# Kernel optimization log

Hardware: AMD Instinct MI355X
Metric: run time of the kernel (lower is better)

The kernel has to match this reference:

```python
import jax, jax.numpy as jnp
import numpy as np

B, T, D, HD, HN, O = 32, 512, 512, 64, 16, 512
EPS = 1e-5


def setup_inputs() -> dict:
    key = jax.random.key(0)
    ks = jax.random.split(key, 12)
    s = lambda fan_in: 1.0 / np.sqrt(fan_in)
    inp = {
        "inputs": jax.random.normal(ks[0], (B, T, D), dtype=jnp.float32),
        "Wq": jax.random.uniform(ks[1], (HN, D, HD), jnp.float32, -s(D), s(D)),
        "bq": jnp.zeros((HN, HD), jnp.float32),
        "Wk": jax.random.uniform(ks[2], (HN, D, HD), jnp.float32, -s(D), s(D)),
        "bk": jnp.zeros((HN, HD), jnp.float32),
        "Wv": jax.random.uniform(ks[3], (HN, D, HD), jnp.float32, -s(D), s(D)),
        "bv": jnp.zeros((HN, HD), jnp.float32),
        "Wr": jax.random.uniform(ks[4], (D, O), jnp.float32, -s(D), s(D)),
        "br": jnp.zeros((O,), jnp.float32),
        "Wo": jax.random.uniform(ks[5], (HN * HD, O), jnp.float32, -s(HN * HD), s(HN * HD)),
        "bo": jnp.zeros((O,), jnp.float32),
        "ln1_w": jnp.ones((O,), jnp.float32),
        "ln1_b": jnp.zeros((O,), jnp.float32),
        "Wfc": jax.random.uniform(ks[6], (O, O), jnp.float32, -s(O), s(O)),
        "bfc": jnp.zeros((O,), jnp.float32),
        "ln2_w": jnp.ones((O,), jnp.float32),
        "ln2_b": jnp.zeros((O,), jnp.float32),
    }
    return inp


def _layernorm(x, w, b):
    mu = jnp.mean(x, axis=-1, keepdims=True)
    var = jnp.mean(jnp.square(x - mu), axis=-1, keepdims=True)
    return (x - mu) * jax.lax.rsqrt(var + EPS) * w + b


def reference(inputs, Wq, bq, Wk, bk, Wv, bv, Wr, br, Wo, bo,
              ln1_w, ln1_b, Wfc, bfc, ln2_w, ln2_b):
    # causal mask: multiply-then-subtract as in the original
    score_mask = jnp.tril(jnp.ones((T, T), jnp.float32))        # [T,T]
    padding_mask = (score_mask == 0).astype(jnp.float32) * 1e9  # [T,T]

    residual = inputs @ Wr + br                                  # [B,T,O]

    # batched per-head projections with nonstandard activations
    q = jax.nn.relu(jnp.einsum('btd,hdf->bhtf', inputs, Wq) + bq[None, :, None, :])
    k = jax.nn.relu(jnp.einsum('btd,hdf->bhtf', inputs, Wk) + bk[None, :, None, :])
    v = jnp.tanh(jnp.einsum('btd,hdf->bhtf', inputs, Wv) + bv[None, :, None, :])

    scores = jnp.einsum('bhtf,bhsf->bhts', q, k) / jnp.sqrt(jnp.float32(HD))
    scores = scores * score_mask - padding_mask                  # [B,H,T,T]
    weights = jax.nn.softmax(scores, axis=-1)
    heads = jnp.einsum('bhts,bhsf->bhtf', weights, v)            # [B,H,T,HD]

    # concat heads (head order preserved) + tanh output projection
    concat = heads.transpose(0, 2, 1, 3).reshape(B, T, HN * HD)
    out = jnp.tanh(concat @ Wo + bo)                             # [B,T,O]

    out = _layernorm(out + residual, ln1_w, ln1_b)
    fc = jax.nn.relu(out @ Wfc + bfc)
    out = _layernorm(fc + out, ln2_w, ln2_b)
    return out
```

## Files before the change

### kernel.cpp

```cpp
#include <hip/hip_runtime.h>
#include <hip/hip_bf16.h>

#define B_  32
#define T_  512
#define D_  512
#define HD_ 64
#define HN_ 16
#define O_  512
#define M_  (B_ * T_)
#define NQ_ (HN_ * HD_)

typedef __bf16 bf16;
typedef __attribute__((ext_vector_type(8))) __bf16 bf16x8;
typedef __attribute__((ext_vector_type(4))) __bf16 bf16x4;
typedef __attribute__((ext_vector_type(4))) float f32x4;

static __device__ __forceinline__ f32x4 mfma16(bf16x8 a, bf16x8 b, f32x4 c) {
    return __builtin_amdgcn_mfma_f32_16x16x32_bf16(a, b, c, 0, 0, 0);
}

static __device__ __forceinline__ void load_lds_16B(const bf16* g, bf16* l) {
    __builtin_amdgcn_global_load_lds(
        (const __attribute__((address_space(1))) unsigned int*)(unsigned long long)g,
        (__attribute__((address_space(3))) unsigned int*)(unsigned long long)l,
        16, 0, 0);
}

static __device__ __forceinline__ float fast_tanh(float x) {
    return 1.f - 2.f / (__expf(2.f * x) + 1.f);
}

static __device__ __forceinline__ int2 swz_block() {
    const int nx = gridDim.x;
    const int nwg = nx * gridDim.y;
    int l = blockIdx.y * nx + blockIdx.x;
    l = (l & 7) * (nwg >> 3) + (l >> 3);
    return make_int2(l % nx, l / nx);
}

__global__ __launch_bounds__(256) void prep_all_kernel(
    const float* __restrict__ inputs,
    const float* __restrict__ Wq, const float* __restrict__ Wk,
    const float* __restrict__ Wv, const float* __restrict__ Wr,
    const float* __restrict__ Wo, const float* __restrict__ Wfc,
    const float* __restrict__ bq, const float* __restrict__ bk,
    const float* __restrict__ bv, const float* __restrict__ br,
    bf16* __restrict__ xin, bf16* __restrict__ wall,
    bf16* __restrict__ wrt, bf16* __restrict__ wot, bf16* __restrict__ wfct,
    float* __restrict__ ball)
{
    __shared__ bf16 tl[64][72];
    const int tid = threadIdx.x;
    int id = blockIdx.x;

    if (id < 4096) {
        const size_t i = ((size_t)id * 256 + tid) * 8;
        f32x4 x0 = *(const f32x4*)(inputs + i);
        f32x4 x1 = *(const f32x4*)(inputs + i + 4);
        bf16x8 v;
        v[0] = (bf16)x0[0]; v[1] = (bf16)x0[1]; v[2] = (bf16)x0[2]; v[3] = (bf16)x0[3];
        v[4] = (bf16)x1[0]; v[5] = (bf16)x1[1]; v[6] = (bf16)x1[2]; v[7] = (bf16)x1[3];
        *(bf16x8*)(xin + i) = v;
        return;
    }
    if (id < 4480) {
        id -= 4096;
        const int kt = id & 7; id >>= 3;
        const int h = id & 15; id >>= 4;
        const float* src = (id == 0) ? Wq : (id == 1) ? Wk : Wv;
        bf16* dst = wall + (size_t)id * (1024 * 512);
        const int k0 = kt * 64;
#pragma unroll
        for (int i = 0; i < 4; i++) {
            const int e = i * 256 + tid;
            const int kk = e >> 4, f4 = (e & 15) * 4;
            const f32x4 v = *(const f32x4*)(src + ((size_t)h * 512 + k0 + kk) * 64 + f4);
#pragma unroll
            for (int j = 0; j < 4; j++) tl[f4 + j][kk] = (bf16)v[j];
        }
        __syncthreads();
#pragma unroll
        for (int i = 0; i < 2; i++) {
            const int e = i * 256 + tid;
            const int f = e >> 3, kc = (e & 7) * 8;
            *(bf16x8*)(dst + ((size_t)h * 64 + f) * 512 + k0 + kc) = *(const bf16x8*)&tl[f][kc];
        }
        return;
    }
    if (id < 4736) {
        id -= 4480;
        const float* src; bf16* dst; int K;
        if (id < 64)       { src = Wr;  dst = wrt;  K = 512;  }
        else if (id < 192) { src = Wo;  dst = wot;  K = 1024; id -= 64; }
        else               { src = Wfc; dst = wfct; K = 512;  id -= 192; }
        const int kt = id >> 3, nt = id & 7;
        const int k0 = kt * 64, n0 = nt * 64;
#pragma unroll
        for (int i = 0; i < 4; i++) {
            const int e = i * 256 + tid;
            const int kk = e >> 4, n4 = (e & 15) * 4;
            const f32x4 v = *(const f32x4*)(src + (size_t)(k0 + kk) * 512 + n0 + n4);
#pragma unroll
            for (int j = 0; j < 4; j++) tl[n4 + j][kk] = (bf16)v[j];
        }
        __syncthreads();
#pragma unroll
        for (int i = 0; i < 2; i++) {
            const int e = i * 256 + tid;
            const int nn = e >> 3, kc = (e & 7) * 8;
            *(bf16x8*)(dst + (size_t)(n0 + nn) * K + k0 + kc) = *(const bf16x8*)&tl[nn][kc];
        }
        return;
    }
    const int i = (id - 4736) * 256 + tid;
    float v = (i < 1024) ? bq[i]
            : (i < 2048) ? bk[i - 1024]
            : (i < 3072) ? bv[i - 2048] : br[i - 3072];
    ball[i] = v;
}

__device__ __forceinline__ void gemm_mainloop_p4(
    const bf16* __restrict__ A, const bf16* __restrict__ Wt,
    const int K, const int m0, const int n0, const int tid,
    bf16* SL, f32x4 (&acc)[4][4])
{
    const int lane = tid & 63;
    const int w = tid >> 6;
    const int wr = w >> 1, wc = w & 1;
    const int lr = lane & 15, lg = lane >> 4;
    const int nt = K >> 5;

    const int r0 = tid >> 2, s0 = tid & 3;
    const int g0 = s0 ^ ((r0 >> 1) & 3);
    const int r1 = r0 + 64;
    const int g1 = s0 ^ ((r1 >> 1) & 3);
    const bf16* aS0 = A + (size_t)(m0 + r0) * K + g0 * 8;
    const bf16* aS1 = A + (size_t)(m0 + r1) * K + g1 * 8;
    const bf16* bS0 = Wt + (size_t)(n0 + r0) * K + g0 * 8;
    const bf16* bS1 = Wt + (size_t)(n0 + r1) * K + g1 * 8;

    auto STAGE = [&](int t) {
        bf16* Ab = SL + (t & 3) * 4096;
        bf16* Bb = SL + 16384 + (t & 3) * 4096;
        const int k0 = t << 5;
        load_lds_16B(aS0 + k0, Ab + tid * 8);
        load_lds_16B(aS1 + k0, Ab + (tid + 256) * 8);
        load_lds_16B(bS0 + k0, Bb + tid * 8);
        load_lds_16B(bS1 + k0, Bb + (tid + 256) * 8);
    };

    STAGE(0); STAGE(1);
    asm volatile("s_waitcnt vmcnt(4)" ::: "memory");
    __builtin_amdgcn_s_barrier();

    for (int t = 0; t < nt; t++) {
        if (t + 2 < nt) {
            STAGE(t + 2);
            asm volatile("s_waitcnt vmcnt(4)" ::: "memory");
        } else {
            asm volatile("s_waitcnt vmcnt(0)" ::: "memory");
        }
        __builtin_amdgcn_s_barrier();

        const bf16* Ab = SL + (t & 3) * 4096;
        const bf16* Bb = SL + 16384 + (t & 3) * 4096;
        bf16x8 a[4], b[4];
#pragma unroll
        for (int mi = 0; mi < 4; mi++) {
            const int row = wr * 64 + mi * 16 + lr;
            a[mi] = *(const bf16x8*)&Ab[row * 32 + ((lg ^ ((row >> 1) & 3)) << 3)];
        }
#pragma unroll
        for (int nj = 0; nj < 4; nj++) {
            const int row = wc * 64 + nj * 16 + lr;
            b[nj] = *(const bf16x8*)&Bb[row * 32 + ((lg ^ ((row >> 1) & 3)) << 3)];
        }
        __builtin_amdgcn_s_setprio(1);
#pragma unroll
        for (int mi = 0; mi < 4; mi++)
#pragma unroll
            for (int nj = 0; nj < 4; nj++)
                acc[mi][nj] = mfma16(a[mi], b[nj], acc[mi][nj]);
        __builtin_amdgcn_s_setprio(0);
    }
    __builtin_amdgcn_s_barrier();
}

template <int ACT>
__device__ __forceinline__ void epi_transpose_store(
    f32x4 (&acc)[4][4], const float* __restrict__ ball, bf16* SL,
    bf16* __restrict__ dst, const int pitch, const int m0, const int nglob0,
    const int nb, const float scale, const int tid)
{
    const int lane = tid & 63, w = tid >> 6;
    const int wr = w >> 1, wc = w & 1, lr = lane & 15, lg = lane >> 4;
#pragma unroll
    for (int mi = 0; mi < 4; mi++) {
#pragma unroll
        for (int nj = 0; nj < 4; nj++) {
            const float bn = ball[nglob0 + wc * 64 + nj * 16 + lr];
            const int rbase = wr * 64 + mi * 16 + lg * 4;
            const int cidx = wc * 64 + nj * 16 + lr;
#pragma unroll
            for (int r = 0; r < 4; r++) {
                float v = acc[mi][nj][r] + bn;
                if constexpr (ACT == 1) v = fmaxf(v, 0.f);
                SL[(rbase + r) * 136 + cidx] = (bf16)(v * scale);
            }
        }
    }
    __syncthreads();
#pragma unroll
    for (int pass = 0; pass < 4; pass++) {
        const int rr = pass * 32 + (tid >> 3);
        const int cc = (tid & 7) * 16;
        bf16x8 v0 = *(const bf16x8*)&SL[rr * 136 + cc];
        bf16x8 v1 = *(const bf16x8*)&SL[rr * 136 + cc + 8];
        *(bf16x8*)(dst + (size_t)(m0 + rr) * pitch + nb + cc) = v0;
        *(bf16x8*)(dst + (size_t)(m0 + rr) * pitch + nb + cc + 8) = v1;
    }
}

__global__ __launch_bounds__(256) void gemm_qkvr_kernel(
    const bf16* __restrict__ A, const bf16* __restrict__ Wall,
    const float* __restrict__ ball,
    bf16* __restrict__ qc, bf16* __restrict__ kb, bf16* __restrict__ vt,
    bf16* __restrict__ resb)
{
    __shared__ bf16 SL[32768];
    const int tid = threadIdx.x;
    const int2 bc = swz_block();
    const int m0 = bc.y * 128, n0 = bc.x * 128;
    f32x4 acc[4][4];
    const f32x4 zero4 = {0.f, 0.f, 0.f, 0.f};
#pragma unroll
    for (int i = 0; i < 4; i++)
#pragma unroll
        for (int j = 0; j < 4; j++) acc[i][j] = zero4;

    gemm_mainloop_p4(A, Wall, 512, m0, n0, tid, SL, acc);

    const int region = n0 >> 10;
    if (region == 0) {
        epi_transpose_store<1>(acc, ball, SL, qc, 1024, m0, n0, n0 & 1023, 0.125f, tid);
    } else if (region == 1) {
        epi_transpose_store<1>(acc, ball, SL, kb, 1024, m0, n0, n0 & 1023, 1.f, tid);
    } else if (region == 3) {
        epi_transpose_store<0>(acc, ball, SL, resb, 512, m0, n0, n0 - 3072, 1.f, tid);
    } else {
        const int lane = tid & 63, w = tid >> 6;
        const int wr = w >> 1, wc = w & 1, lr = lane & 15, lg = lane >> 4;
#pragma unroll
        for (int mi = 0; mi < 4; mi++) {
#pragma unroll
            for (int nj = 0; nj < 4; nj++) {
                const int n = n0 + wc * 64 + nj * 16 + lr;
                const float bn = ball[n];
                const int m = m0 + wr * 64 + mi * 16 + lg * 4;
                const int bb = m >> 9, t = m & 511;
                const int nn = n - 2048, hh = nn >> 6, f = nn & 63;
                bf16x4 st;
#pragma unroll
                for (int r = 0; r < 4; r++) st[r] = (bf16)fast_tanh(acc[mi][nj][r] + bn);
                *(bf16x4*)(vt + (((size_t)(bb * 16 + hh) * 64 + f) << 9) + t) = st;
            }
        }
    }
}

template <int ACT>
__global__ __launch_bounds__(256) void gemm_std_kernel(
    const bf16* __restrict__ A, const bf16* __restrict__ Wt,
    const float* __restrict__ bias, bf16* __restrict__ C, const int K)
{
    __shared__ bf16 SL[32768];
    const int tid = threadIdx.x;
    const int2 bc = swz_block();
    const int m0 = bc.y * 128, n0 = bc.x * 128;
    f32x4 acc[4][4];
    const f32x4 zero4 = {0.f, 0.f, 0.f, 0.f};
#pragma unroll
    for (int i = 0; i < 4; i++)
#pragma unroll
        for (int j = 0; j < 4; j++) acc[i][j] = zero4;

    gemm_mainloop_p4(A, Wt, K, m0, n0, tid, SL, acc);

    const int lane = tid & 63, w = tid >> 6;
    const int wr = w >> 1, wc = w & 1, lr = lane & 15, lg = lane >> 4;
#pragma unroll
    for (int mi = 0; mi < 4; mi++) {
#pragma unroll
        for (int nj = 0; nj < 4; nj++) {
            const float bn = bias[n0 + wc * 64 + nj * 16 + lr];
            const int rbase = wr * 64 + mi * 16 + lg * 4;
            const int cidx = wc * 64 + nj * 16 + lr;
#pragma unroll
            for (int r = 0; r < 4; r++) {
                float v = acc[mi][nj][r] + bn;
                if constexpr (ACT == 1) v = fmaxf(v, 0.f);
                else if constexpr (ACT == 2) v = fast_tanh(v);
                SL[(rbase + r) * 136 + cidx] = (bf16)v;
            }
        }
    }
    __syncthreads();
#pragma unroll
    for (int pass = 0; pass < 4; pass++) {
        const int rr = pass * 32 + (tid >> 3);
        const int cc = (tid & 7) * 16;
        bf16x8 v0 = *(const bf16x8*)&SL[rr * 136 + cc];
        bf16x8 v1 = *(const bf16x8*)&SL[rr * 136 + cc + 8];
        *(bf16x8*)(C + (size_t)(m0 + rr) * 512 + n0 + cc) = v0;
        *(bf16x8*)(C + (size_t)(m0 + rr) * 512 + n0 + cc + 8) = v1;
    }
}

static __device__ __forceinline__ int sigma_k(int t) {
    return (t & 32) | ((t & 4) << 2) | ((t & 24) >> 1) | (t & 3);
}

__global__ __launch_bounds__(256) void mfma_attn_kernel(
    const bf16* __restrict__ Kb, const bf16* __restrict__ Vt, bf16* __restrict__ QC)
{
    __shared__ bf16 Ks[2][64][72];
    __shared__ bf16 Vts[2][64][72];

    int l = blockIdx.x;
    l = (l & 7) * 256 + (l >> 3);
    const int qb = l & 3;
    const int h = (l >> 2) & 15;
    const int b = l >> 6;
    const int tid = threadIdx.x;
    const int lane = tid & 63;
    const int w = tid >> 6;
    const int lr = lane & 15, lg = lane >> 4;

    const int qrow0 = qb * 128 + w * 32;
    const size_t qbase = ((size_t)b * T_ + qrow0) * NQ_ + h * 64;
    const int bh = b * HN_ + h;

    bf16x8 qf[2][2];
#pragma unroll
    for (int mi = 0; mi < 2; mi++)
#pragma unroll
        for (int kc = 0; kc < 2; kc++)
            qf[mi][kc] = *(const bf16x8*)(QC + qbase + (size_t)(mi * 16 + lr) * NQ_ + kc * 32 + lg * 8);

    const f32x4 zero4 = {0.f, 0.f, 0.f, 0.f};
    f32x4 o[2][4];
    float m_st[2] = {-1e30f, -1e30f}, l_st[2] = {0.f, 0.f};
#pragma unroll
    for (int mi = 0; mi < 2; mi++)
#pragma unroll
        for (int dj = 0; dj < 4; dj++) o[mi][dj] = zero4;

    const int nsb = 2 * qb + 2;

    bf16x8 kreg[2], vreg[2];
    auto LOADR = [&](int sb) {
#pragma unroll
        for (int i = 0; i < 2; i++) {
            const int ci = i * 256 + tid, row = ci >> 3, cc = ci & 7;
            kreg[i] = *(const bf16x8*)(Kb + ((size_t)b * T_ + sb * 64 + row) * NQ_ + h * 64 + cc * 8);
            vreg[i] = *(const bf16x8*)(Vt + ((size_t)bh * 64 + row) * T_ + sb * 64 + cc * 8);
        }
    };
    auto WRITE = [&](int buf) {
#pragma unroll
        for (int i = 0; i < 2; i++) {
            const int ci = i * 256 + tid, row = ci >> 3, cc = ci & 7;
            *(bf16x8*)&Ks[buf][sigma_k(row)][cc * 8] = kreg[i];
            *(bf16x8*)&Vts[buf][row][cc * 8] = vreg[i];
        }
    };

    LOADR(0); WRITE(0); __syncthreads();
    int cur = 0;

    for (int sb = 0; sb < nsb; sb++) {
        const bool pf = (sb + 1 < nsb);
        if (pf) LOADR(sb + 1);

        if (sb * 64 <= qrow0 + 31) {
            f32x4 sc[2][4];
#pragma unroll
            for (int mi = 0; mi < 2; mi++)
#pragma unroll
                for (int nj = 0; nj < 4; nj++) sc[mi][nj] = zero4;
            __builtin_amdgcn_s_setprio(1);
#pragma unroll
            for (int kc = 0; kc < 2; kc++) {
                bf16x8 kf[4];
#pragma unroll
                for (int nj = 0; nj < 4; nj++)
                    kf[nj] = *(const bf16x8*)&Ks[cur][nj * 16 + lr][kc * 32 + lg * 8];
#pragma unroll
                for (int mi = 0; mi < 2; mi++)
#pragma unroll
                    for (int nj = 0; nj < 4; nj++)
                        sc[mi][nj] = mfma16(kf[nj], qf[mi][kc], sc[mi][nj]);
            }
            __builtin_amdgcn_s_setprio(0);
            const bool needmask = (sb * 64 + 63 > qrow0);
            float tm[2];
#pragma unroll
            for (int mi = 0; mi < 2; mi++) {
                const int qg = qrow0 + mi * 16 + lr;
                float mx = -1e30f;
#pragma unroll
                for (int nj = 0; nj < 4; nj++) {
                    const int kvb = sb * 64 + ((nj >> 1) << 5) + ((nj & 1) << 2) + lg * 8;
#pragma unroll
                    for (int r = 0; r < 4; r++) {
                        float s = sc[mi][nj][r];
                        if (needmask && (kvb + r > qg)) s = -1e30f;
                        sc[mi][nj][r] = s;
                        mx = fmaxf(mx, s);
                    }
                }
                mx = fmaxf(mx, __shfl_xor(mx, 16));
                mx = fmaxf(mx, __shfl_xor(mx, 32));
                tm[mi] = mx;
            }
            const bool defer = (tm[0] <= m_st[0] + 8.f) && (tm[1] <= m_st[1] + 8.f);
            if (!__all(defer)) {
#pragma unroll
                for (int mi = 0; mi < 2; mi++) {
                    const float mn = fmaxf(m_st[mi], tm[mi]);
                    const float sf = __expf(m_st[mi] - mn);
                    m_st[mi] = mn;
                    l_st[mi] *= sf;
#pragma unroll
                    for (int dj = 0; dj < 4; dj++)
#pragma unroll
                        for (int r = 0; r < 4; r++) o[mi][dj][r] *= sf;
                }
            }
            bf16x4 pk[2][4];
#pragma unroll
            for (int mi = 0; mi < 2; mi++) {
                float ts = 0.f;
#pragma unroll
                for (int nj = 0; nj < 4; nj++)
#pragma unroll
                    for (int r = 0; r < 4; r++) {
                        const float p = __expf(sc[mi][nj][r] - m_st[mi]);
                        ts += p;
                        pk[mi][nj][r] = (bf16)p;
                    }
                ts += __shfl_xor(ts, 16);
                ts += __shfl_xor(ts, 32);
                l_st[mi] += ts;
            }
            __builtin_amdgcn_s_setprio(1);
#pragma unroll
            for (int kc = 0; kc < 2; kc++) {
                bf16x8 vf[4], pf2[2];
#pragma unroll
                for (int mi = 0; mi < 2; mi++) {
                    bf16x8 t;
#pragma unroll
                    for (int r = 0; r < 4; r++) { t[r] = pk[mi][2 * kc][r]; t[r + 4] = pk[mi][2 * kc + 1][r]; }
                    pf2[mi] = t;
                }
#pragma unroll
                for (int dj = 0; dj < 4; dj++)
                    vf[dj] = *(const bf16x8*)&Vts[cur][dj * 16 + lr][kc * 32 + lg * 8];
#pragma unroll
                for (int mi = 0; mi < 2; mi++)
#pragma unroll
                    for (int dj = 0; dj < 4; dj++)
                        o[mi][dj] = mfma16(vf[dj], pf2[mi], o[mi][dj]);
            }
            __builtin_amdgcn_s_setprio(0);
        }

        if (pf) WRITE(cur ^ 1);
        __syncthreads();
        cur ^= 1;
    }

#pragma unroll
    for (int mi = 0; mi < 2; mi++) {
        const float inv = 1.f / l_st[mi];
        const size_t rowoff = qbase + (size_t)(mi * 16 + lr) * NQ_;
#pragma unroll
        for (int dj = 0; dj < 4; dj++) {
            bf16x4 st;
#pragma unroll
            for (int r = 0; r < 4; r++) st[r] = (bf16)(o[mi][dj][r] * inv);
            *(bf16x4*)(QC + rowoff + dj * 16 + lg * 4) = st;
        }
    }
}

template <bool F32OUT>
__global__ __launch_bounds__(256) void ln_kernel(
    const bf16* __restrict__ xa, const bf16* __restrict__ xb,
    const float* __restrict__ w, const float* __restrict__ bias,
    void* __restrict__ outv)
{
    const int row = blockIdx.x * 4 + (threadIdx.x >> 6);
    const int ln = threadIdx.x & 63;
    const size_t base = (size_t)row * 512 + ln * 8;
    const bf16x8 va = *(const bf16x8*)(xa + base);
    const bf16x8 vb = *(const bf16x8*)(xb + base);
    float x[8];
    float s = 0.f;
#pragma unroll
    for (int i = 0; i < 8; i++) { x[i] = (float)va[i] + (float)vb[i]; s += x[i]; }
#pragma unroll
    for (int off = 32; off >= 1; off >>= 1) s += __shfl_xor(s, off);
    const float mean = s * (1.f / 512.f);
    float ss = 0.f;
#pragma unroll
    for (int i = 0; i < 8; i++) { x[i] -= mean; ss += x[i] * x[i]; }
#pragma unroll
    for (int off = 32; off >= 1; off >>= 1) ss += __shfl_xor(ss, off);
    const float inv = rsqrtf(ss * (1.f / 512.f) + 1e-5f);
    const f32x4 w0 = *(const f32x4*)(w + ln * 8);
    const f32x4 w1 = *(const f32x4*)(w + ln * 8 + 4);
    const f32x4 b0 = *(const f32x4*)(bias + ln * 8);
    const f32x4 b1 = *(const f32x4*)(bias + ln * 8 + 4);
    if constexpr (F32OUT) {
        f32x4 y0, y1;
#pragma unroll
        for (int i = 0; i < 4; i++) {
            y0[i] = x[i] * inv * w0[i] + b0[i];
            y1[i] = x[4 + i] * inv * w1[i] + b1[i];
        }
        *(f32x4*)((float*)outv + base) = y0;
        *(f32x4*)((float*)outv + base + 4) = y1;
    } else {
        bf16x8 y;
#pragma unroll
        for (int i = 0; i < 4; i++) {
            y[i] = (bf16)(x[i] * inv * w0[i] + b0[i]);
            y[4 + i] = (bf16)(x[4 + i] * inv * w1[i] + b1[i]);
        }
        *(bf16x8*)((bf16*)outv + base) = y;
    }
}

extern "C" void kernel_launch(void* const* d_in, const int* in_sizes, int n_in,
                              void* d_out, int out_size, void* d_ws, size_t ws_size,
                              hipStream_t stream)
{
    const float* inputs = (const float*)d_in[0];
    const float* Wq = (const float*)d_in[1];
    const float* bq = (const float*)d_in[2];
    const float* Wk = (const float*)d_in[3];
    const float* bk = (const float*)d_in[4];
    const float* Wv = (const float*)d_in[5];
    const float* bv = (const float*)d_in[6];
    const float* Wr = (const float*)d_in[7];
    const float* br = (const float*)d_in[8];
    const float* Wo = (const float*)d_in[9];
    const float* bo = (const float*)d_in[10];
    const float* ln1w = (const float*)d_in[11];
    const float* ln1b = (const float*)d_in[12];
    const float* Wfc = (const float*)d_in[13];
    const float* bfc = (const float*)d_in[14];
    const float* ln2w = (const float*)d_in[15];
    const float* ln2b = (const float*)d_in[16];
    float* out = (float*)d_out;

    const size_t MB = 1024ull * 1024ull;
    char* ws = (char*)d_ws;
    bf16* qc   = (bf16*)(ws);
    bf16* kb   = (bf16*)(ws + 32 * MB);
    bf16* vt   = (bf16*)(ws + 64 * MB);
    bf16* xin  = (bf16*)(ws + 96 * MB);
    bf16* wall = (bf16*)(ws + 112 * MB);
    bf16* wot  = (bf16*)(ws + 112 * MB + 3670016);
    bf16* wfct = (bf16*)(ws + 112 * MB + 3670016 + 1048576);
    float* ball = (float*)(ws + 112 * MB + 3670016 + 1048576 + 524288);
    bf16* wrt  = wall + (size_t)3072 * 512;
    bf16* resb = (bf16*)d_out;
    bf16* att  = kb;
    bf16* ln1  = kb + (size_t)8 * MB;
    bf16* fcb  = vt;

    const dim3 blk(256);

    prep_all_kernel<<<dim3(4750), blk, 0, stream>>>(
        inputs, Wq, Wk, Wv, Wr, Wo, Wfc, bq, bk, bv, br,
        xin, wall, wrt, wot, wfct, ball);

    gemm_qkvr_kernel<<<dim3(28, 128), blk, 0, stream>>>(xin, wall, ball, qc, kb, vt, resb);
    mfma_attn_kernel<<<dim3(B_ * HN_ * 4), blk, 0, stream>>>(kb, vt, qc);
    gemm_std_kernel<2><<<dim3(4, 128), blk, 0, stream>>>(qc, wot, bo, att, 1024);
    ln_kernel<false><<<dim3(4096), blk, 0, stream>>>(att, resb, ln1w, ln1b, ln1);
    gemm_std_kernel<1><<<dim3(4, 128), blk, 0, stream>>>(ln1, wfct, bfc, fcb, 512);
    ln_kernel<true ><<<dim3(4096), blk, 0, stream>>>(fcb, ln1, ln2w, ln2b, out);
}
```

Measured before the change: 241.5 us.

## Use 256x256 tiles with 4-stage pipeline for fused QKV/residual projection GEMM

```diff
diff --git a/kernel.cpp b/kernel.cpp
--- a/kernel.cpp
+++ b/kernel.cpp
@@ -119,6 +119,150 @@
     ball[i] = v;
 }
 
+__global__ __launch_bounds__(512, 2) void gemm_qkvr256_kernel(
+    const bf16* __restrict__ A, const bf16* __restrict__ Wall,
+    const float* __restrict__ ball,
+    bf16* __restrict__ qc, bf16* __restrict__ kb, bf16* __restrict__ vt,
+    bf16* __restrict__ resb)
+{
+    __shared__ bf16 SL[65536];
+    const int tid = threadIdx.x;
+    const int lane = tid & 63;
+    const int w = tid >> 6;
+    const int wm = w >> 2, wn = w & 3;
+    const int lr = lane & 15, lg = lane >> 4;
+    const int K = 512;
+
+    const int2 bc = swz_block();
+    const int m0 = bc.y * 256, n0 = bc.x * 256;
+
+    const int srow = tid >> 2;
+    const int g0 = (tid & 3) ^ ((srow >> 1) & 3);
+    const bf16* aP = A + (size_t)(m0 + srow) * K + g0 * 8;
+    const bf16* bP = Wall + (size_t)(n0 + srow) * K + g0 * 8;
+
+    auto STAGE = [&](int t) {
+        bf16* Ab = SL + (t & 3) * 8192;
+        bf16* Bb = SL + 32768 + (t & 3) * 8192;
+        const int k0 = t << 5;
+        load_lds_16B(aP + k0, Ab + tid * 8);
+        load_lds_16B(aP + k0 + (size_t)128 * K, Ab + (512 + tid) * 8);
+        load_lds_16B(bP + k0, Bb + tid * 8);
+        load_lds_16B(bP + k0 + (size_t)128 * K, Bb + (512 + tid) * 8);
+    };
+
+    f32x4 acc[8][4];
+    const f32x4 zero4 = {0.f, 0.f, 0.f, 0.f};
+#pragma unroll
+    for (int i = 0; i < 8; i++)
+#pragma unroll
+        for (int j = 0; j < 4; j++) acc[i][j] = zero4;
+
+    STAGE(0); STAGE(1); STAGE(2);
+
+    for (int t = 0; t < 16; t++) {
+        if (t <= 13)      asm volatile("s_waitcnt vmcnt(8)" ::: "memory");
+        else if (t == 14) asm volatile("s_waitcnt vmcnt(4)" ::: "memory");
+        else              asm volatile("s_waitcnt vmcnt(0)" ::: "memory");
+        asm volatile("s_barrier" ::: "memory");
+
+        const bf16* Ab = SL + (t & 3) * 8192;
+        const bf16* Bb = SL + 32768 + (t & 3) * 8192;
+
+        bf16x8 bfr[4], afr[4];
+#pragma unroll
+        for (int nj = 0; nj < 4; nj++) {
+            const int row = wn * 64 + nj * 16 + lr;
+            bfr[nj] = *(const bf16x8*)&Bb[row * 32 + ((lg ^ ((row >> 1) & 3)) << 3)];
+        }
+#pragma unroll
+        for (int mi = 0; mi < 4; mi++) {
+            const int row = wm * 128 + mi * 16 + lr;
+            afr[mi] = *(const bf16x8*)&Ab[row * 32 + ((lg ^ ((row >> 1) & 3)) << 3)];
+        }
+        if (t <= 12) STAGE(t + 3);
+        __builtin_amdgcn_s_setprio(1);
+#pragma unroll
+        for (int mi = 0; mi < 4; mi++)
+#pragma unroll
+            for (int nj = 0; nj < 4; nj++)
+                acc[mi][nj] = mfma16(afr[mi], bfr[nj], acc[mi][nj]);
+        __builtin_amdgcn_s_setprio(0);
+        asm volatile("s_barrier" ::: "memory");
+
+#pragma unroll
+        for (int mi = 0; mi < 4; mi++) {
+            const int row = wm * 128 + (mi + 4) * 16 + lr;
+            afr[mi] = *(const bf16x8*)&Ab[row * 32 + ((lg ^ ((row >> 1) & 3)) << 3)];
+        }
+        __builtin_amdgcn_s_setprio(1);
+#pragma unroll
+        for (int mi = 0; mi < 4; mi++)
+#pragma unroll
+            for (int nj = 0; nj < 4; nj++)
+                acc[mi + 4][nj] = mfma16(afr[mi], bfr[nj], acc[mi + 4][nj]);
+        __builtin_amdgcn_s_setprio(0);
+    }
+    __syncthreads();
+
+    const int region = n0 >> 10;
+    if (region == 2) {
+#pragma unroll
+        for (int mi = 0; mi < 8; mi++) {
+#pragma unroll
+            for (int nj = 0; nj < 4; nj++) {
+                const int n = n0 + wn * 64 + nj * 16 + lr;
+                const float bn = ball[n];
+                const int m = m0 + wm * 128 + mi * 16 + lg * 4;
+                const int bb = m >> 9, tt = m & 511;
+                const int nn = n - 2048, hh = nn >> 6, f = nn & 63;
+                bf16x4 st;
+#pragma unroll
+                for (int r = 0; r < 4; r++) st[r] = (bf16)fast_tanh(acc[mi][nj][r] + bn);
+                *(bf16x4*)(vt + (((size_t)(bb * 16 + hh) * 64 + f) << 9) + tt) = st;
+            }
+        }
+    } else {
+        bf16* dst; int pitch, nb; float scale = 1.f; bool rl = false;
+        if (region == 0)      { dst = qc;   pitch = 1024; nb = n0;        scale = 0.125f; rl = true; }
+        else if (region == 1) { dst = kb;   pitch = 1024; nb = n0 - 1024; rl = true; }
+        else                  { dst = resb; pitch = 512;  nb = n0 - 3072; }
+        float bn[4];
+#pragma unroll
+        for (int nj = 0; nj < 4; nj++) bn[nj] = ball[n0 + wn * 64 + nj * 16 + lr];
+#pragma unroll
+        for (int half = 0; half < 2; half++) {
+            if (wm == half) {
+#pragma unroll
+                for (int mi = 0; mi < 8; mi++) {
+#pragma unroll
+                    for (int nj = 0; nj < 4; nj++) {
+                        const int col = wn * 64 + nj * 16 + lr;
+#pragma unroll
+                        for (int r = 0; r < 4; r++) {
+                            float v = acc[mi][nj][r] + bn[nj];
+                            if (rl) v = fmaxf(v, 0.f);
+                            SL[(mi * 16 + lg * 4 + r) * 264 + col] = (bf16)(v * scale);
+                        }
+                    }
+                }
+            }
+            __syncthreads();
+#pragma unroll
+            for (int i = 0; i < 4; i++) {
+                const int rr = i * 32 + (tid >> 4);
+                const int cc = (tid & 15) * 16;
+                bf16x8 v0 = *(const bf16x8*)&SL[rr * 264 + cc];
+                bf16x8 v1 = *(const bf16x8*)&SL[rr * 264 + cc + 8];
+                bf16* p = dst + (size_t)(m0 + half * 128 + rr) * pitch + nb + cc;
+                *(bf16x8*)p = v0;
+                *(bf16x8*)(p + 8) = v1;
+            }
+            __syncthreads();
+        }
+    }
+}
+
 __device__ __forceinline__ void gemm_mainloop_p4(
     const bf16* __restrict__ A, const bf16* __restrict__ Wt,
     const int K, const int m0, const int n0, const int tid,
@@ -184,88 +328,6 @@
         __builtin_amdgcn_s_setprio(0);
     }
     __builtin_amdgcn_s_barrier();
-}
-
-template <int ACT>
-__device__ __forceinline__ void epi_transpose_store(
-    f32x4 (&acc)[4][4], const float* __restrict__ ball, bf16* SL,
-    bf16* __restrict__ dst, const int pitch, const int m0, const int nglob0,
-    const int nb, const float scale, const int tid)
-{
-    const int lane = tid & 63, w = tid >> 6;
-    const int wr = w >> 1, wc = w & 1, lr = lane & 15, lg = lane >> 4;
-#pragma unroll
-    for (int mi = 0; mi < 4; mi++) {
-#pragma unroll
-        for (int nj = 0; nj < 4; nj++) {
-            const float bn = ball[nglob0 + wc * 64 + nj * 16 + lr];
-            const int rbase = wr * 64 + mi * 16 + lg * 4;
-            const int cidx = wc * 64 + nj * 16 + lr;
-#pragma unroll
-            for (int r = 0; r < 4; r++) {
-                float v = acc[mi][nj][r] + bn;
-                if constexpr (ACT == 1) v = fmaxf(v, 0.f);
-                SL[(rbase + r) * 136 + cidx] = (bf16)(v * scale);
-            }
-        }
-    }
-    __syncthreads();
-#pragma unroll
-    for (int pass = 0; pass < 4; pass++) {
-        const int rr = pass * 32 + (tid >> 3);
-        const int cc = (tid & 7) * 16;
-        bf16x8 v0 = *(const bf16x8*)&SL[rr * 136 + cc];
-        bf16x8 v1 = *(const bf16x8*)&SL[rr * 136 + cc + 8];
-        *(bf16x8*)(dst + (size_t)(m0 + rr) * pitch + nb + cc) = v0;
-        *(bf16x8*)(dst + (size_t)(m0 + rr) * pitch + nb + cc + 8) = v1;
-    }
-}
-
-__global__ __launch_bounds__(256) void gemm_qkvr_kernel(
-    const bf16* __restrict__ A, const bf16* __restrict__ Wall,
-    const float* __restrict__ ball,
-    bf16* __restrict__ qc, bf16* __restrict__ kb, bf16* __restrict__ vt,
-    bf16* __restrict__ resb)
-{
-    __shared__ bf16 SL[32768];
-    const int tid = threadIdx.x;
-    const int2 bc = swz_block();
-    const int m0 = bc.y * 128, n0 = bc.x * 128;
-    f32x4 acc[4][4];
-    const f32x4 zero4 = {0.f, 0.f, 0.f, 0.f};
-#pragma unroll
-    for (int i = 0; i < 4; i++)
-#pragma unroll
-        for (int j = 0; j < 4; j++) acc[i][j] = zero4;
-
-    gemm_mainloop_p4(A, Wall, 512, m0, n0, tid, SL, acc);
-
-    const int region = n0 >> 10;
-    if (region == 0) {
-        epi_transpose_store<1>(acc, ball, SL, qc, 1024, m0, n0, n0 & 1023, 0.125f, tid);
-    } else if (region == 1) {
-        epi_transpose_store<1>(acc, ball, SL, kb, 1024, m0, n0, n0 & 1023, 1.f, tid);
-    } else if (region == 3) {
-        epi_transpose_store<0>(acc, ball, SL, resb, 512, m0, n0, n0 - 3072, 1.f, tid);
-    } else {
-        const int lane = tid & 63, w = tid >> 6;
-        const int wr = w >> 1, wc = w & 1, lr = lane & 15, lg = lane >> 4;
-#pragma unroll
-        for (int mi = 0; mi < 4; mi++) {
-#pragma unroll
-            for (int nj = 0; nj < 4; nj++) {
-                const int n = n0 + wc * 64 + nj * 16 + lr;
-                const float bn = ball[n];
-                const int m = m0 + wr * 64 + mi * 16 + lg * 4;
-                const int bb = m >> 9, t = m & 511;
-                const int nn = n - 2048, hh = nn >> 6, f = nn & 63;
-                bf16x4 st;
-#pragma unroll
-                for (int r = 0; r < 4; r++) st[r] = (bf16)fast_tanh(acc[mi][nj][r] + bn);
-                *(bf16x4*)(vt + (((size_t)(bb * 16 + hh) * 64 + f) << 9) + t) = st;
-            }
-        }
-    }
 }
 
 template <int ACT>
@@ -588,7 +650,8 @@
         inputs, Wq, Wk, Wv, Wr, Wo, Wfc, bq, bk, bv, br,
         xin, wall, wrt, wot, wfct, ball);
 
-    gemm_qkvr_kernel<<<dim3(28, 128), blk, 0, stream>>>(xin, wall, ball, qc, kb, vt, resb);
+    gemm_qkvr256_kernel<<<dim3(14, 64), dim3(512), 0, stream>>>(
+        xin, wall, ball, qc, kb, vt, resb);
     mfma_attn_kernel<<<dim3(B_ * HN_ * 4), blk, 0, stream>>>(kb, vt, qc);
     gemm_std_kernel<2><<<dim3(4, 128), blk, 0, stream>>>(qc, wot, bo, att, 1024);
     ln_kernel<false><<<dim3(4096), blk, 0, stream>>>(att, resb, ln1w, ln1b, ln1);
```

After: 251.5 us. +4.2%, slower.
